# Kernel optimization log

Hardware: AMD Instinct MI355X
Metric: run time of the kernel (lower is better)

The kernel has to match this reference:

```python
import jax, jax.numpy as jnp
import numpy as np

N = 10000      # nodes
E = 80000      # directed edges (before self loops)
F_IN = 128     # input feature dim
OUT = 16       # out_channels (classes)


def setup_inputs() -> dict:
    key = jax.random.key(0)
    ks = jax.random.split(key, 20)
    p = lambda k, shape: (jax.random.normal(k, shape, jnp.float32) * 0.1)
    x = jax.random.normal(ks[0], (N, F_IN), jnp.float32)
    edge_index = jax.random.randint(ks[1], (2, E), 0, N, dtype=jnp.int64)
    return {
        "x": x, "edge_index": edge_index,
        # conv1: in=128 -> heads=10, ch=256
        "W1": p(ks[2], (F_IN, 10 * 256)), "as1": p(ks[3], (10, 256)), "ad1": p(ks[4], (10, 256)), "b1": jnp.zeros((10 * 256,), jnp.float32),
        # conv2: in=2560 -> heads=8, ch=56
        "W2": p(ks[5], (2560, 8 * 56)), "as2": p(ks[6], (8, 56)), "ad2": p(ks[7], (8, 56)), "b2": jnp.zeros((8 * 56,), jnp.float32),
        # conv3: in=448 -> heads=4, ch=32
        "W3": p(ks[8], (448, 4 * 32)), "as3": p(ks[9], (4, 32)), "ad3": p(ks[10], (4, 32)), "b3": jnp.zeros((4 * 32,), jnp.float32),
        # conv4: in=128 -> heads=1, ch=OUT, concat=False (mean over heads)
        "W4": p(ks[11], (128, 1 * OUT)), "as4": p(ks[12], (1, OUT)), "ad4": p(ks[13], (1, OUT)), "b4": jnp.zeros((OUT,), jnp.float32),
    }


def _gat_layer(x, src, dst, W, a_src, a_dst, b, heads, ch, concat, n):
    # linear projection -> [n, H, C]
    h = (x @ W).reshape(n, heads, ch)
    # per-node attention halves (PyG decomposition of a^T [h_i || h_j])
    e_src = jnp.einsum('nhc,hc->nh', h, a_src)
    e_dst = jnp.einsum('nhc,hc->nh', h, a_dst)
    # per-edge logits, LeakyReLU(0.2) as in PyG GATConv
    e = jax.nn.leaky_relu(e_src[src] + e_dst[dst], 0.2)  # [E', H]
    # segment softmax over edges grouped by destination node
    m = jax.ops.segment_max(e, dst, num_segments=n)
    m = jnp.where(jnp.isfinite(m), m, 0.0)
    ex = jnp.exp(e - m[dst])
    denom = jax.ops.segment_sum(ex, dst, num_segments=n)
    alpha = ex / (denom[dst] + 1e-16)  # [E', H]
    # weighted scatter-sum of source messages
    out = jax.ops.segment_sum(alpha[:, :, None] * h[src], dst, num_segments=n)  # [n, H, C]
    out = out.reshape(n, heads * ch) if concat else out.mean(axis=1)
    return out + b


def reference(x, edge_index, W1, as1, ad1, b1, W2, as2, ad2, b2,
              W3, as3, ad3, b3, W4, as4, ad4, b4):
    n = x.shape[0]
    loops = jnp.arange(n, dtype=edge_index.dtype)
    src = jnp.concatenate([edge_index[0], loops])  # add_self_loops=True
    dst = jnp.concatenate([edge_index[1], loops])
    lrelu = lambda t: jax.nn.leaky_relu(t, 0.1)  # outer activations in forward()
    h = lrelu(_gat_layer(x, src, dst, W1, as1, ad1, b1, 10, 256, True, n))
    h = lrelu(_gat_layer(h, src, dst, W2, as2, ad2, b2, 8, 56, True, n))
    h = lrelu(_gat_layer(h, src, dst, W3, as3, ad3, b3, 4, 32, True, n))
    h = lrelu(_gat_layer(h, src, dst, W4, as4, ad4, b4, 1, OUT, False, n))
    return jax.nn.softmax(h, axis=1)
```

## Files before the change

kernel.cpp:

```cpp
#include <hip/hip_runtime.h>
#include <math.h>

#define NNODES 10000
#define MPAD   10112
#define NEDGES 80000
#define ETOT   (NEDGES + NNODES)

typedef __attribute__((ext_vector_type(4))) float f32x4;
typedef __attribute__((ext_vector_type(8))) short bf16x8;
typedef __attribute__((ext_vector_type(4))) unsigned int u32x4;

__device__ inline unsigned short f2bf(float f) {
    unsigned int u = __float_as_uint(f);
    unsigned int r = (u + 0x7fffu + ((u >> 16) & 1u)) >> 16;
    return (unsigned short)r;
}
__device__ inline float bf2f(unsigned short h) {
    return __uint_as_float(((unsigned int)h) << 16);
}
__device__ inline float lrelu01(float v) { return (v > 0.f) ? v : 0.1f * v; }
__device__ inline float lrelu02(float v) { return (v > 0.f) ? v : 0.2f * v; }

__global__ void count_deg(const int* __restrict__ ei, int* __restrict__ indeg,
                          int E, int n) {
    int i = blockIdx.x * blockDim.x + threadIdx.x;
    if (i >= E + n) return;
    int dst = (i < E) ? ei[E + i] : (i - E);
    atomicAdd(&indeg[dst], 1);
}

__global__ void scan_rowptr(const int* __restrict__ indeg, int* __restrict__ row_ptr,
                            int* __restrict__ cursor, int n) {
    __shared__ int sums[1024];
    int tid = threadIdx.x;
    int per = (n + 1023) / 1024;
    int start = tid * per;
    int end = start + per; if (end > n) end = n;
    int s = 0;
    for (int i = start; i < end; ++i) s += indeg[i];
    sums[tid] = s;
    __syncthreads();
    for (int off = 1; off < 1024; off <<= 1) {
        int v = (tid >= off) ? sums[tid - off] : 0;
        __syncthreads();
        sums[tid] += v;
        __syncthreads();
    }
    int excl = (tid == 0) ? 0 : sums[tid - 1];
    for (int i = start; i < end; ++i) {
        row_ptr[i] = excl;
        cursor[i]  = excl;
        excl += indeg[i];
    }
    if (tid == 1023) row_ptr[n] = sums[1023];
}

__global__ void scatter_edges(const int* __restrict__ ei, int* __restrict__ cursor,
                              int* __restrict__ col, int E, int n) {
    int i = blockIdx.x * blockDim.x + threadIdx.x;
    if (i >= E + n) return;
    int src, dst;
    if (i < E) { src = ei[i]; dst = ei[E + i]; }
    else       { src = i - E; dst = i - E; }
    int pos = atomicAdd(&cursor[dst], 1);
    col[pos] = src;
}

__global__ void convert_bf16(const float* __restrict__ in, unsigned short* __restrict__ out,
                             int n) {
    int i = blockIdx.x * blockDim.x + threadIdx.x;
    if (i < n) out[i] = f2bf(in[i]);
}

__global__ void transpose_all(const float* __restrict__ W1, const float* __restrict__ W2,
                              const float* __restrict__ W3,
                              unsigned short* __restrict__ W1t,
                              unsigned short* __restrict__ W2t,
                              unsigned short* __restrict__ W3t) {
    __shared__ float t[32][33];
    int b = blockIdx.x;
    const float* W; unsigned short* Wt; int K, N, nb, kb;
    if (b < 320)       { W = W1; Wt = W1t; K = 128;  N = 2560; int i = b;        nb = i % 80; kb = i / 80; }
    else if (b < 1440) { W = W2; Wt = W2t; K = 2560; N = 448;  int i = b - 320;  nb = i % 14; kb = i / 14; }
    else               { W = W3; Wt = W3t; K = 448;  N = 128;  int i = b - 1440; nb = i % 4;  kb = i / 4;  }
    int kb32 = kb * 32, nb32 = nb * 32;
    int tx = threadIdx.x, ty = threadIdx.y;
    #pragma unroll
    for (int i = 0; i < 32; i += 8)
        t[ty + i][tx] = W[(size_t)(kb32 + ty + i) * N + nb32 + tx];
    __syncthreads();
    #pragma unroll
    for (int i = 0; i < 32; i += 8)
        Wt[(size_t)(nb32 + ty + i) * K + kb32 + tx] = f2bf(t[tx][ty + i]);
}

__global__ void make_wsd(const float* __restrict__ W1, const float* __restrict__ as1,
                         const float* __restrict__ ad1,
                         float* __restrict__ wsrc, float* __restrict__ wdst) {
    int idx = blockIdx.x * blockDim.x + threadIdx.x;
    if (idx >= 1280) return;
    int h = idx >> 7, k = idx & 127;
    const float* wrow = W1 + (size_t)k * 2560 + h * 256;
    const float* as = as1 + h * 256;
    const float* ad = ad1 + h * 256;
    float s = 0.f, d = 0.f;
    for (int c = 0; c < 256; c += 4) {
        f32x4 w = *(const f32x4*)&wrow[c];
        f32x4 a = *(const f32x4*)&as[c];
        f32x4 b = *(const f32x4*)&ad[c];
        #pragma unroll
        for (int j = 0; j < 4; ++j) { s += w[j] * a[j]; d += w[j] * b[j]; }
    }
    wsrc[h * 128 + k] = s;
    wdst[h * 128 + k] = d;
}

__global__ __launch_bounds__(256) void e1_dots(const unsigned short* __restrict__ xb,
                                               const float* __restrict__ wsrc,
                                               const float* __restrict__ wdst,
                                               float* __restrict__ e_src,
                                               float* __restrict__ e_dst, int M) {
    __shared__ float ws[1280], wd[1280];
    int tid = threadIdx.x;
    for (int i = tid; i < 1280; i += 256) { ws[i] = wsrc[i]; wd[i] = wdst[i]; }
    __syncthreads();
    int node = blockIdx.x * 4 + (tid >> 6);
    int lane = tid & 63;
    if (node >= M) return;
    unsigned int xv = ((const unsigned int*)xb)[node * 64 + lane];
    float v0 = bf2f((unsigned short)(xv & 0xffffu));
    float v1 = bf2f((unsigned short)(xv >> 16));
    #pragma unroll
    for (int h = 0; h < 10; ++h) {
        float ps = v0 * ws[h * 128 + 2 * lane] + v1 * ws[h * 128 + 2 * lane + 1];
        float pd = v0 * wd[h * 128 + 2 * lane] + v1 * wd[h * 128 + 2 * lane + 1];
        #pragma unroll
        for (int off = 32; off; off >>= 1) {
            ps += __shfl_down(ps, off);
            pd += __shfl_down(pd, off);
        }
        if (lane == 0) { e_src[node * 10 + h] = ps; e_dst[node * 10 + h] = pd; }
    }
}

__global__ __launch_bounds__(64) void agg_x(const unsigned short* __restrict__ xb,
                                            const float* __restrict__ e_src,
                                            const float* __restrict__ e_dst,
                                            const int* __restrict__ row_ptr,
                                            const int* __restrict__ col,
                                            unsigned short* __restrict__ xagg) {
    int node = blockIdx.x;
    int lane = threadIdx.x;
    int rs = row_ptr[node], re = row_ptr[node + 1];
    float edv = (lane < 10) ? e_dst[node * 10 + lane] : 0.f;

    float dn = 0.f;
    float a0[10], a1[10];
    #pragma unroll
    for (int h = 0; h < 10; ++h) { a0[h] = 0.f; a1[h] = 0.f; }
    for (int i = rs; i < re; ++i) {
        int s = col[i];
        float w = 0.f;
        if (lane < 10) w = __expf(lrelu02(e_src[s * 10 + lane] + edv));
        dn += w;
        unsigned int xv = ((const unsigned int*)xb)[s * 64 + lane];
        float v0 = bf2f((unsigned short)(xv & 0xffffu));
        float v1 = bf2f((unsigned short)(xv >> 16));
        #pragma unroll
        for (int h = 0; h < 10; ++h) {
            float wh = __shfl(w, h);
            a0[h] += wh * v0;
            a1[h] += wh * v1;
        }
    }
    #pragma unroll
    for (int h = 0; h < 10; ++h) {
        float rdn = 1.f / (__shfl(dn, h) + 1e-16f);
        unsigned int o = (unsigned int)f2bf(a0[h] * rdn) |
                         ((unsigned int)f2bf(a1[h] * rdn) << 16);
        ((unsigned int*)xagg)[((size_t)node * 10 + h) * 64 + lane] = o;
    }
}


#define GBM 128
#define GBK 32
__global__ __launch_bounds__(256) void gemm_l1(const unsigned short* __restrict__ A,
                                               const unsigned short* __restrict__ Bt,
                                               const float* __restrict__ bias,
                                               unsigned short* __restrict__ C) {
    constexpr int NT = 128, NI = 4, K = 128;
    __shared__ short As[GBM * GBK];
    __shared__ short Bs[NT * GBK];
    int h  = blockIdx.x >> 1;
    int nt = blockIdx.x & 1;
    int bn = h * 256 + nt * 128;
    int bm = blockIdx.y * GBM;
    int tid  = threadIdx.x;
    int wave = tid >> 6, lane = tid & 63;
    int wr = wave >> 1, wc = wave & 1;
    int lrow  = lane >> 2;
    int lk    = (((lane & 3) ^ ((lrow >> 1) & 3))) * 8;
    int row16 = lane & 15;
    int qs    = (((lane >> 4) ^ ((row16 >> 1) & 3))) * 8;

    f32x4 acc[4][NI];
    #pragma unroll
    for (int mi = 0; mi < 4; ++mi)
        #pragma unroll
        for (int ni = 0; ni < NI; ++ni) acc[mi][ni] = (f32x4){0.f, 0.f, 0.f, 0.f};

    for (int k0 = 0; k0 < K; k0 += GBK) {
        #pragma unroll
        for (int i = 0; i < 2; ++i) {
            int c = i * 4 + wave;
            int row = c * 16 + lrow;
            const unsigned short* gp = A + ((size_t)(bm + row) * 10 + h) * K + k0 + lk;
            __builtin_amdgcn_global_load_lds(
                (const __attribute__((address_space(1))) void*)gp,
                (__attribute__((address_space(3))) void*)&As[c * 512], 16, 0, 0);
        }
        #pragma unroll
        for (int i = 0; i < 2; ++i) {
            int c = i * 4 + wave;
            int row = c * 16 + lrow;
            const unsigned short* gp = Bt + (size_t)(bn + row) * K + k0 + lk;
            __builtin_amdgcn_global_load_lds(
                (const __attribute__((address_space(1))) void*)gp,
                (__attribute__((address_space(3))) void*)&Bs[c * 512], 16, 0, 0);
        }
        __syncthreads();
        bf16x8 af[4], bfr[NI];
        #pragma unroll
        for (int mi = 0; mi < 4; ++mi)
            af[mi] = *(const bf16x8*)&As[(wr * 64 + mi * 16 + row16) * GBK + qs];
        #pragma unroll
        for (int ni = 0; ni < NI; ++ni)
            bfr[ni] = *(const bf16x8*)&Bs[(wc * 64 + ni * 16 + row16) * GBK + qs];
        #pragma unroll
        for (int mi = 0; mi < 4; ++mi)
            #pragma unroll
            for (int ni = 0; ni < NI; ++ni)
                acc[mi][ni] = __builtin_amdgcn_mfma_f32_16x16x32_bf16(
                    af[mi], bfr[ni], acc[mi][ni], 0, 0, 0);
        __syncthreads();
    }

    int rbase = bm + wr * 64 + (lane >> 4) * 4;
    #pragma unroll
    for (int mi = 0; mi < 4; ++mi)
        #pragma unroll
        for (int ni = 0; ni < NI; ++ni) {
            int cc = bn + wc * 64 + ni * 16 + (lane & 15);
            float b = bias[cc];
            #pragma unroll
            for (int r = 0; r < 4; ++r) {
                float v = lrelu01(acc[mi][ni][r] + b);
                C[(size_t)(rbase + mi * 16 + r) * 2560 + cc] = f2bf(v);
            }
        }
}

template <int NT, bool SWIZ>
__global__ __launch_bounds__(256) void gemm_mfma(const unsigned short* __restrict__ A,
                                                 const unsigned short* __restrict__ Bt,
                                                 unsigned short* __restrict__ C,
                                                 int N, int nbn, int K, int klen) {
    constexpr int NI = NT / 32;
    __shared__ short As[GBM * GBK];
    __shared__ short Bs[NT * GBK];
    int bn, bm, kbeg, kend;
    size_t zoff = 0;
    if constexpr (SWIZ) {
        int b = blockIdx.x;
        int x = b & 7, t = b >> 3;
        int j = x + 8 * (t / nbn);
        if (j >= MPAD / GBM) return;
        bn = (t % nbn) * NT;
        bm = j * GBM;
        kbeg = blockIdx.y * klen;
        kend = kbeg + klen;
        zoff = (size_t)blockIdx.y * MPAD * N;
    } else {
        bn = blockIdx.x * NT;
        bm = blockIdx.y * GBM;
        kbeg = 0; kend = K;
    }
    int tid  = threadIdx.x;
    int wave = tid >> 6, lane = tid & 63;
    int wr = wave >> 1, wc = wave & 1;
    int lrow  = lane >> 2;
    int lk    = (((lane & 3) ^ ((lrow >> 1) & 3))) * 8;
    int row16 = lane & 15;
    int qs    = (((lane >> 4) ^ ((row16 >> 1) & 3))) * 8;

    f32x4 acc[4][NI];
    #pragma unroll
    for (int mi = 0; mi < 4; ++mi)
        #pragma unroll
        for (int ni = 0; ni < NI; ++ni) acc[mi][ni] = (f32x4){0.f, 0.f, 0.f, 0.f};

    for (int k0 = kbeg; k0 < kend; k0 += GBK) {
        #pragma unroll
        for (int i = 0; i < 2; ++i) {
            int c = i * 4 + wave;
            int row = c * 16 + lrow;
            const unsigned short* gp = A + (size_t)(bm + row) * K + k0 + lk;
            __builtin_amdgcn_global_load_lds(
                (const __attribute__((address_space(1))) void*)gp,
                (__attribute__((address_space(3))) void*)&As[c * 512], 16, 0, 0);
        }
        #pragma unroll
        for (int i = 0; i < NT / 64; ++i) {
            int c = i * 4 + wave;
            int row = c * 16 + lrow;
            const unsigned short* gp = Bt + (size_t)(bn + row) * K + k0 + lk;
            __builtin_amdgcn_global_load_lds(
                (const __attribute__((address_space(1))) void*)gp,
                (__attribute__((address_space(3))) void*)&Bs[c * 512], 16, 0, 0);
        }
        __syncthreads();
        bf16x8 af[4], bfr[NI];
        #pragma unroll
        for (int mi = 0; mi < 4; ++mi)
            af[mi] = *(const bf16x8*)&As[(wr * 64 + mi * 16 + row16) * GBK + qs];
        #pragma unroll
        for (int ni = 0; ni < NI; ++ni)
            bfr[ni] = *(const bf16x8*)&Bs[(wc * (NT / 2) + ni * 16 + row16) * GBK + qs];
        #pragma unroll
        for (int mi = 0; mi < 4; ++mi)
            #pragma unroll
            for (int ni = 0; ni < NI; ++ni)
                acc[mi][ni] = __builtin_amdgcn_mfma_f32_16x16x32_bf16(
                    af[mi], bfr[ni], acc[mi][ni], 0, 0, 0);
        __syncthreads();
    }

    int rbase = bm + wr * 64 + (lane >> 4) * 4;
    int cbase = bn + wc * (NT / 2) + (lane & 15);
    #pragma unroll
    for (int mi = 0; mi < 4; ++mi)
        #pragma unroll
        for (int ni = 0; ni < NI; ++ni)
            #pragma unroll
            for (int r = 0; r < 4; ++r)
                C[zoff + (size_t)(rbase + mi * 16 + r) * N + cbase + ni * 16] =
                    f2bf(acc[mi][ni][r]);
}

template <int S>
__global__ void reduce_k(const unsigned int* __restrict__ P, unsigned int* __restrict__ out,
                         size_t stride, int n2) {
    int i = blockIdx.x * blockDim.x + threadIdx.x;
    if (i >= n2) return;
    float lo = 0.f, hi = 0.f;
    #pragma unroll
    for (int s = 0; s < S; ++s) {
        unsigned int v = P[s * stride + i];
        lo += bf2f((unsigned short)(v & 0xffffu));
        hi += bf2f((unsigned short)(v >> 16));
    }
    out[i] = (unsigned int)f2bf(lo) | ((unsigned int)f2bf(hi) << 16);
}

__global__ __launch_bounds__(256) void gemm4_attn(const unsigned short* __restrict__ A,
                                                  const float* __restrict__ W,
                                                  const float* __restrict__ as4,
                                                  const float* __restrict__ ad4,
                                                  unsigned short* __restrict__ C,
                                                  float* __restrict__ e_src,
                                                  float* __restrict__ e_dst, int M) {
    __shared__ float Ws[128 * 16];
    int tid = threadIdx.x;
    for (int i = tid; i < 2048; i += 256) Ws[i] = W[i];
    __syncthreads();
    int node = blockIdx.x * 16 + (tid >> 4);
    int n = tid & 15;
    if (node >= M) return;
    const unsigned short* ap = A + (size_t)node * 128;
    float acc = 0.f;
    #pragma unroll 8
    for (int k = 0; k < 128; ++k)
        acc += bf2f(ap[k]) * Ws[k * 16 + n];
    C[(size_t)node * 16 + n] = f2bf(acc);
    float vs = acc * as4[n];
    float vd = acc * ad4[n];
    #pragma unroll
    for (int off = 1; off < 16; off <<= 1) {
        vs += __shfl_xor(vs, off);
        vd += __shfl_xor(vd, off);
    }
    if (n == 0) { e_src[node] = vs; e_dst[node] = vd; }
}

template <int H, int C>
__global__ __launch_bounds__(64) void attn_small(const unsigned short* __restrict__ h,
                                                 const float* __restrict__ a_src,
                                                 const float* __restrict__ a_dst,
                                                 float* __restrict__ e_src,
                                                 float* __restrict__ e_dst) {
    constexpr int LPH = 64 / H;
    constexpr int CPL = C / LPH;
    int node = blockIdx.x;
    int lane = threadIdx.x;
    int head = lane / LPH;
    int k = lane - head * LPH;
    const unsigned short* hp = h + (size_t)node * (H * C) + head * C + k * CPL;
    const float* as = a_src + head * C + k * CPL;
    const float* ad = a_dst + head * C + k * CPL;
    float s1 = 0.f, s2 = 0.f;
    #pragma unroll
    for (int c = 0; c < CPL; ++c) {
        float v = bf2f(hp[c]);
        s1 += v * as[c];
        s2 += v * ad[c];
    }
    #pragma unroll
    for (int off = LPH / 2; off; off >>= 1) {
        s1 += __shfl_down(s1, off);
        s2 += __shfl_down(s2, off);
    }
    if (k == 0) { e_src[node * H + head] = s1; e_dst[node * H + head] = s2; }
}

__global__ __launch_bounds__(64) void agg_l2(const unsigned short* __restrict__ h,
                                             const float* __restrict__ e_src,
                                             const float* __restrict__ e_dst,
                                             const int* __restrict__ row_ptr,
                                             const int* __restrict__ col,
                                             const float* __restrict__ bias,
                                             unsigned short* __restrict__ out) {
    const int H = 8;
    int node = blockIdx.x;
    int lane = threadIdx.x;
    bool act = lane < 56;
    int head = act ? (lane / 7) : 0;
    int cpos = act ? (lane - head * 7) : 0;
    int rs = row_ptr[node], re = row_ptr[node + 1];
    float edv = e_dst[node * H + head];

    float dn = 0.f;
    float acc0[8], acc1[8];
    #pragma unroll
    for (int k = 0; k < 8; ++k) { acc0[k] = 0.f; acc1[k] = 0.f; }
    int i = rs;
    for (; i + 1 < re; i += 2) {
        int s0 = col[i], s1 = col[i + 1];
        float es0 = e_src[s0 * H + head];
        float es1 = e_src[s1 * H + head];
        u32x4 hv0 = *(const u32x4*)(h + (size_t)s0 * 448 + head * 56 + cpos * 8);
        u32x4 hv1 = *(const u32x4*)(h + (size_t)s1 * 448 + head * 56 + cpos * 8);
        float w0 = __expf(lrelu02(es0 + edv));
        float w1 = __expf(lrelu02(es1 + edv));
        dn += w0 + w1;
        #pragma unroll
        for (int d = 0; d < 4; ++d) {
            acc0[2 * d]     += w0 * bf2f((unsigned short)(hv0[d] & 0xffffu));
            acc0[2 * d + 1] += w0 * bf2f((unsigned short)(hv0[d] >> 16));
            acc1[2 * d]     += w1 * bf2f((unsigned short)(hv1[d] & 0xffffu));
            acc1[2 * d + 1] += w1 * bf2f((unsigned short)(hv1[d] >> 16));
        }
    }
    if (i < re) {
        int s = col[i];
        float w = __expf(lrelu02(e_src[s * H + head] + edv));
        dn += w;
        u32x4 hv = *(const u32x4*)(h + (size_t)s * 448 + head * 56 + cpos * 8);
        #pragma unroll
        for (int d = 0; d < 4; ++d) {
            acc0[2 * d]     += w * bf2f((unsigned short)(hv[d] & 0xffffu));
            acc0[2 * d + 1] += w * bf2f((unsigned short)(hv[d] >> 16));
        }
    }
    float rdn = 1.f / (dn + 1e-16f);

    if (act) {
        const float* bp = bias + head * 56 + cpos * 8;
        u32x4 o;
        #pragma unroll
        for (int d = 0; d < 4; ++d) {
            float v0 = lrelu01((acc0[2 * d] + acc1[2 * d]) * rdn + bp[2 * d]);
            float v1 = lrelu01((acc0[2 * d + 1] + acc1[2 * d + 1]) * rdn + bp[2 * d + 1]);
            o[d] = (unsigned int)f2bf(v0) | ((unsigned int)f2bf(v1) << 16);
        }
        *(u32x4*)(out + (size_t)node * 448 + head * 56 + cpos * 8) = o;
    }
}

__global__ __launch_bounds__(64) void agg_l3(const unsigned short* __restrict__ h,
                                             const float* __restrict__ e_src,
                                             const float* __restrict__ e_dst,
                                             const int* __restrict__ row_ptr,
                                             const int* __restrict__ col,
                                             const float* __restrict__ bias,
                                             unsigned short* __restrict__ out) {
    const int H = 4;
    int node = blockIdx.x;
    int lane = threadIdx.x;
    bool act = lane < 16;
    int head = (lane >> 2) & 3;
    int cpos = lane & 3;
    int rs = row_ptr[node], re = row_ptr[node + 1];
    float edv = e_dst[node * H + head];

    float dn = 0.f;
    float acc0[8], acc1[8];
    #pragma unroll
    for (int k = 0; k < 8; ++k) { acc0[k] = 0.f; acc1[k] = 0.f; }
    int i = rs;
    for (; i + 1 < re; i += 2) {
        int s0 = col[i], s1 = col[i + 1];
        float es0 = e_src[s0 * H + head];
        float es1 = e_src[s1 * H + head];
        u32x4 hv0 = *(const u32x4*)(h + (size_t)s0 * 128 + head * 32 + cpos * 8);
        u32x4 hv1 = *(const u32x4*)(h + (size_t)s1 * 128 + head * 32 + cpos * 8);
        float w0 = __expf(lrelu02(es0 + edv));
        float w1 = __expf(lrelu02(es1 + edv));
        dn += w0 + w1;
        #pragma unroll
        for (int d = 0; d < 4; ++d) {
            acc0[2 * d]     += w0 * bf2f((unsigned short)(hv0[d] & 0xffffu));
            acc0[2 * d + 1] += w0 * bf2f((unsigned short)(hv0[d] >> 16));
            acc1[2 * d]     += w1 * bf2f((unsigned short)(hv1[d] & 0xffffu));
            acc1[2 * d + 1] += w1 * bf2f((unsigned short)(hv1[d] >> 16));
        }
    }
    if (i < re) {
        int s = col[i];
        float w = __expf(lrelu02(e_src[s * H + head] + edv));
        dn += w;
        u32x4 hv = *(const u32x4*)(h + (size_t)s * 128 + head * 32 + cpos * 8);
        #pragma unroll
        for (int d = 0; d < 4; ++d) {
            acc0[2 * d]     += w * bf2f((unsigned short)(hv[d] & 0xffffu));
            acc0[2 * d + 1] += w * bf2f((unsigned short)(hv[d] >> 16));
        }
    }
    float rdn = 1.f / (dn + 1e-16f);

    if (act) {
        const float* bp = bias + head * 32 + cpos * 8;
        u32x4 o;
        #pragma unroll
        for (int d = 0; d < 4; ++d) {
            float v0 = lrelu01((acc0[2 * d] + acc1[2 * d]) * rdn + bp[2 * d]);
            float v1 = lrelu01((acc0[2 * d + 1] + acc1[2 * d + 1]) * rdn + bp[2 * d + 1]);
            o[d] = (unsigned int)f2bf(v0) | ((unsigned int)f2bf(v1) << 16);
        }
        *(u32x4*)(out + (size_t)node * 128 + head * 32 + cpos * 8) = o;
    }
}

__global__ __launch_bounds__(64) void agg4_softmax(const unsigned int* __restrict__ h2,
                                                   const float* __restrict__ e_src,
                                                   const float* __restrict__ e_dst,
                                                   const int* __restrict__ row_ptr,
                                                   const int* __restrict__ col,
                                                   const float* __restrict__ bias,
                                                   float* __restrict__ out) {
    int node = blockIdx.x;
    int lane = threadIdx.x;
    int cpos = lane & 7;
    int rs = row_ptr[node], re = row_ptr[node + 1];
    float edv = e_dst[node];

    float dn = 0.f, a0 = 0.f, a1 = 0.f;
    for (int i = rs; i < re; ++i) {
        int s = col[i];
        float w = __expf(lrelu02(e_src[s] + edv));
        dn += w;
        unsigned int hv = h2[(size_t)s * 8 + cpos];
        a0 += w * bf2f((unsigned short)(hv & 0xffffu));
        a1 += w * bf2f((unsigned short)(hv >> 16));
    }
    float rdn = 1.f / (dn + 1e-16f);
    float v0 = lrelu01(a0 * rdn + bias[2 * cpos]);
    float v1 = lrelu01(a1 * rdn + bias[2 * cpos + 1]);

    float m = fmaxf(v0, v1);
    #pragma unroll
    for (int off = 4; off; off >>= 1) m = fmaxf(m, __shfl_xor(m, off));
    float e0 = __expf(v0 - m), e1 = __expf(v1 - m);
    float s = e0 + e1;
    #pragma unroll
    for (int off = 4; off; off >>= 1) s += __shfl_xor(s, off);
    float r = 1.f / s;
    if (lane < 8) {
        out[node * 16 + 2 * cpos]     = e0 * r;
        out[node * 16 + 2 * cpos + 1] = e1 * r;
    }
}

extern "C" void kernel_launch(void* const* d_in, const int* in_sizes, int n_in,
                              void* d_out, int out_size, void* d_ws, size_t ws_size,
                              hipStream_t stream) {
    const float* x   = (const float*)d_in[0];
    const int*   ei  = (const int*)d_in[1];
    const float* W1  = (const float*)d_in[2];
    const float* as1 = (const float*)d_in[3];
    const float* ad1 = (const float*)d_in[4];
    const float* b1  = (const float*)d_in[5];
    const float* W2  = (const float*)d_in[6];
    const float* as2 = (const float*)d_in[7];
    const float* ad2 = (const float*)d_in[8];
    const float* b2  = (const float*)d_in[9];
    const float* W3  = (const float*)d_in[10];
    const float* as3 = (const float*)d_in[11];
    const float* ad3 = (const float*)d_in[12];
    const float* b3  = (const float*)d_in[13];
    const float* W4  = (const float*)d_in[14];
    const float* as4 = (const float*)d_in[15];
    const float* ad4 = (const float*)d_in[16];
    const float* b4  = (const float*)d_in[17];

    char* ws = (char*)d_ws;
    size_t off = 0;
    auto alloc = [&](size_t bytes) -> void* {
        void* p = ws + off;
        off = (off + bytes + 255) & ~(size_t)255;
        return p;
    };
    unsigned short* hbuf = (unsigned short*)alloc((size_t)MPAD * 2560 * sizeof(short));
    unsigned short* abuf = (unsigned short*)alloc((size_t)MPAD * 2560 * sizeof(short));
    unsigned short* pbuf = (unsigned short*)alloc((size_t)4 * MPAD * 448 * sizeof(short));
    unsigned short* xagg = (unsigned short*)alloc((size_t)MPAD * 10 * 128 * sizeof(short));
    unsigned short* W1t  = (unsigned short*)alloc((size_t)2560 * 128 * sizeof(short));
    unsigned short* W2t  = (unsigned short*)alloc((size_t)448 * 2560 * sizeof(short));
    unsigned short* W3t  = (unsigned short*)alloc((size_t)128 * 448 * sizeof(short));
    float* wsrc   = (float*)alloc((size_t)10 * 128 * sizeof(float));
    float* wdst   = (float*)alloc((size_t)10 * 128 * sizeof(float));
    float* e_src  = (float*)alloc((size_t)NNODES * 10 * sizeof(float));
    float* e_dst  = (float*)alloc((size_t)NNODES * 10 * sizeof(float));
    int* indeg    = (int*)alloc(NNODES * sizeof(int));
    int* row_ptr  = (int*)alloc((NNODES + 1) * sizeof(int));
    int* cursor   = (int*)alloc(NNODES * sizeof(int));
    int* col      = (int*)alloc(ETOT * sizeof(int));
    (void)ws_size;

    hipMemsetAsync(indeg, 0, NNODES * sizeof(int), stream);
    int eb = (ETOT + 255) / 256;
    count_deg<<<eb, 256, 0, stream>>>(ei, indeg, NEDGES, NNODES);
    scan_rowptr<<<1, 1024, 0, stream>>>(indeg, row_ptr, cursor, NNODES);
    scatter_edges<<<eb, 256, 0, stream>>>(ei, cursor, col, NEDGES, NNODES);

    transpose_all<<<1496, dim3(32, 8), 0, stream>>>(W1, W2, W3, W1t, W2t, W3t);
    make_wsd<<<20, 64, 0, stream>>>(W1, as1, ad1, wsrc, wdst);
    convert_bf16<<<(NNODES * 128 + 255) / 256, 256, 0, stream>>>(x, abuf, NNODES * 128);

    const int Mb = MPAD / GBM;

    e1_dots<<<(NNODES + 3) / 4, 256, 0, stream>>>(abuf, wsrc, wdst, e_src, e_dst, NNODES);
    agg_x<<<NNODES, 64, 0, stream>>>(abuf, e_src, e_dst, row_ptr, col, xagg);
    gemm_l1<<<dim3(20, Mb), 256, 0, stream>>>(xagg, W1t, b1, abuf);

    gemm_mfma<64, true><<<dim3(8 * 7 * 10, 4), 256, 0, stream>>>(
        abuf, W2t, pbuf, 448, 7, 2560, 640);
    {
        int n2 = NNODES * 448 / 2;
        reduce_k<4><<<(n2 + 255) / 256, 256, 0, stream>>>(
            (const unsigned int*)pbuf, (unsigned int*)hbuf, (size_t)MPAD * 448 / 2, n2);
    }
    attn_small<8, 56><<<NNODES, 64, 0, stream>>>(hbuf, as2, ad2, e_src, e_dst);
    agg_l2<<<NNODES, 64, 0, stream>>>(hbuf, e_src, e_dst, row_ptr, col, b2, abuf);

    gemm_mfma<64, true><<<dim3(8 * 2 * 10, 2), 256, 0, stream>>>(
        abuf, W3t, pbuf, 128, 2, 448, 224);
    {
        int n2 = NNODES * 128 / 2;
        reduce_k<2><<<(n2 + 255) / 256, 256, 0, stream>>>(
            (const unsigned int*)pbuf, (unsigned int*)hbuf, (size_t)MPAD * 128 / 2, n2);
    }
    attn_small<4, 32><<<NNODES, 64, 0, stream>>>(hbuf, as3, ad3, e_src, e_dst);
    agg_l3<<<NNODES, 64, 0, stream>>>(hbuf, e_src, e_dst, row_ptr, col, b3, abuf);

    gemm4_attn<<<(NNODES + 15) / 16, 256, 0, stream>>>(
        abuf, W4, as4, ad4, hbuf, e_src, e_dst, NNODES);
    agg4_softmax<<<NNODES, 64, 0, stream>>>(
        (const unsigned int*)hbuf, e_src, e_dst, row_ptr, col, b4, (float*)d_out);
}
```

Baseline: 299.8 us.

## Merge prep kernels, widen GEMM K-tile to 64, fuse split-K reduce with attention

```diff
diff --git a/kernel.cpp b/kernel.cpp
--- a/kernel.cpp
+++ b/kernel.cpp
@@ -21,12 +21,71 @@
 __device__ inline float lrelu01(float v) { return (v > 0.f) ? v : 0.1f * v; }
 __device__ inline float lrelu02(float v) { return (v > 0.f) ? v : 0.2f * v; }
 
-__global__ void count_deg(const int* __restrict__ ei, int* __restrict__ indeg,
-                          int E, int n) {
-    int i = blockIdx.x * blockDim.x + threadIdx.x;
-    if (i >= E + n) return;
-    int dst = (i < E) ? ei[E + i] : (i - E);
-    atomicAdd(&indeg[dst], 1);
+__global__ __launch_bounds__(256) void prep_all(const int* __restrict__ ei,
+                                                int* __restrict__ indeg,
+                                                const float* __restrict__ x,
+                                                unsigned short* __restrict__ xb,
+                                                const float* __restrict__ W1,
+                                                const float* __restrict__ as1,
+                                                const float* __restrict__ ad1,
+                                                float* __restrict__ wsrc,
+                                                float* __restrict__ wdst,
+                                                const float* __restrict__ W2,
+                                                const float* __restrict__ W3,
+                                                unsigned short* __restrict__ W1t,
+                                                unsigned short* __restrict__ W2t,
+                                                unsigned short* __restrict__ W3t) {
+    __shared__ float t[32][33];
+    int b = blockIdx.x, tid = threadIdx.x;
+    if (b < 352) {
+        int i = b * 256 + tid;
+        if (i < ETOT) {
+            int dst = (i < NEDGES) ? ei[NEDGES + i] : (i - NEDGES);
+            atomicAdd(&indeg[dst], 1);
+        }
+        return;
+    }
+    b -= 352;
+    if (b < 5000) {
+        int i = b * 256 + tid;
+        if (i < NNODES * 128) xb[i] = f2bf(x[i]);
+        return;
+    }
+    b -= 5000;
+    if (b < 5) {
+        int idx = b * 256 + tid;
+        if (idx < 1280) {
+            int h = idx >> 7, k = idx & 127;
+            const float* wrow = W1 + (size_t)k * 2560 + h * 256;
+            const float* as = as1 + h * 256;
+            const float* ad = ad1 + h * 256;
+            float s = 0.f, d = 0.f;
+            for (int c = 0; c < 256; c += 4) {
+                f32x4 w = *(const f32x4*)&wrow[c];
+                f32x4 a = *(const f32x4*)&as[c];
+                f32x4 bb = *(const f32x4*)&ad[c];
+                #pragma unroll
+                for (int j = 0; j < 4; ++j) { s += w[j] * a[j]; d += w[j] * bb[j]; }
+            }
+            wsrc[h * 128 + k] = s;
+            wdst[h * 128 + k] = d;
+        }
+        return;
+    }
+    b -= 5;
+    const float* W; unsigned short* Wt; int K, N, nb, kb;
+    if (b < 320)       { W = W1; Wt = W1t; K = 128;  N = 2560; nb = b % 80; kb = b / 80; }
+    else if (b < 1440) { W = W2; Wt = W2t; K = 2560; N = 448;  int i = b - 320;  nb = i % 14; kb = i / 14; }
+    else               { W = W3; Wt = W3t; K = 448;  N = 128;  int i = b - 1440; nb = i % 4;  kb = i / 4;  }
+    int kb32 = kb * 32, nb32 = nb * 32;
+    int tx = tid & 31, ty = tid >> 5;
+    #pragma unroll
+    for (int i = 0; i < 32; i += 8)
+        t[ty + i][tx] = W[(size_t)(kb32 + ty + i) * N + nb32 + tx];
+    __syncthreads();
+    #pragma unroll
+    for (int i = 0; i < 32; i += 8)
+        Wt[(size_t)(nb32 + ty + i) * K + kb32 + tx] = f2bf(t[tx][ty + i]);
 }
 
 __global__ void scan_rowptr(const int* __restrict__ indeg, int* __restrict__ row_ptr,
@@ -55,78 +114,33 @@
     if (tid == 1023) row_ptr[n] = sums[1023];
 }
 
-__global__ void scatter_edges(const int* __restrict__ ei, int* __restrict__ cursor,
-                              int* __restrict__ col, int E, int n) {
-    int i = blockIdx.x * blockDim.x + threadIdx.x;
-    if (i >= E + n) return;
-    int src, dst;
-    if (i < E) { src = ei[i]; dst = ei[E + i]; }
-    else       { src = i - E; dst = i - E; }
-    int pos = atomicAdd(&cursor[dst], 1);
-    col[pos] = src;
-}
-
-__global__ void convert_bf16(const float* __restrict__ in, unsigned short* __restrict__ out,
-                             int n) {
-    int i = blockIdx.x * blockDim.x + threadIdx.x;
-    if (i < n) out[i] = f2bf(in[i]);
-}
-
-__global__ void transpose_all(const float* __restrict__ W1, const float* __restrict__ W2,
-                              const float* __restrict__ W3,
-                              unsigned short* __restrict__ W1t,
-                              unsigned short* __restrict__ W2t,
-                              unsigned short* __restrict__ W3t) {
-    __shared__ float t[32][33];
-    int b = blockIdx.x;
-    const float* W; unsigned short* Wt; int K, N, nb, kb;
-    if (b < 320)       { W = W1; Wt = W1t; K = 128;  N = 2560; int i = b;        nb = i % 80; kb = i / 80; }
-    else if (b < 1440) { W = W2; Wt = W2t; K = 2560; N = 448;  int i = b - 320;  nb = i % 14; kb = i / 14; }
-    else               { W = W3; Wt = W3t; K = 448;  N = 128;  int i = b - 1440; nb = i % 4;  kb = i / 4;  }
-    int kb32 = kb * 32, nb32 = nb * 32;
-    int tx = threadIdx.x, ty = threadIdx.y;
-    #pragma unroll
-    for (int i = 0; i < 32; i += 8)
-        t[ty + i][tx] = W[(size_t)(kb32 + ty + i) * N + nb32 + tx];
-    __syncthreads();
-    #pragma unroll
-    for (int i = 0; i < 32; i += 8)
-        Wt[(size_t)(nb32 + ty + i) * K + kb32 + tx] = f2bf(t[tx][ty + i]);
-}
-
-__global__ void make_wsd(const float* __restrict__ W1, const float* __restrict__ as1,
-                         const float* __restrict__ ad1,
-                         float* __restrict__ wsrc, float* __restrict__ wdst) {
-    int idx = blockIdx.x * blockDim.x + threadIdx.x;
-    if (idx >= 1280) return;
-    int h = idx >> 7, k = idx & 127;
-    const float* wrow = W1 + (size_t)k * 2560 + h * 256;
-    const float* as = as1 + h * 256;
-    const float* ad = ad1 + h * 256;
-    float s = 0.f, d = 0.f;
-    for (int c = 0; c < 256; c += 4) {
-        f32x4 w = *(const f32x4*)&wrow[c];
-        f32x4 a = *(const f32x4*)&as[c];
-        f32x4 b = *(const f32x4*)&ad[c];
-        #pragma unroll
-        for (int j = 0; j < 4; ++j) { s += w[j] * a[j]; d += w[j] * b[j]; }
-    }
-    wsrc[h * 128 + k] = s;
-    wdst[h * 128 + k] = d;
-}
-
-__global__ __launch_bounds__(256) void e1_dots(const unsigned short* __restrict__ xb,
-                                               const float* __restrict__ wsrc,
-                                               const float* __restrict__ wdst,
-                                               float* __restrict__ e_src,
-                                               float* __restrict__ e_dst, int M) {
+__global__ __launch_bounds__(256) void scatter_e1(const int* __restrict__ ei,
+                                                  int* __restrict__ cursor,
+                                                  int* __restrict__ col,
+                                                  const unsigned short* __restrict__ xb,
+                                                  const float* __restrict__ wsrc,
+                                                  const float* __restrict__ wdst,
+                                                  float* __restrict__ e_src,
+                                                  float* __restrict__ e_dst) {
     __shared__ float ws[1280], wd[1280];
-    int tid = threadIdx.x;
+    int b = blockIdx.x, tid = threadIdx.x;
+    if (b < 352) {
+        int i = b * 256 + tid;
+        if (i < ETOT) {
+            int src, dst;
+            if (i < NEDGES) { src = ei[i]; dst = ei[NEDGES + i]; }
+            else            { src = i - NEDGES; dst = i - NEDGES; }
+            int pos = atomicAdd(&cursor[dst], 1);
+            col[pos] = src;
+        }
+        return;
+    }
+    b -= 352;
     for (int i = tid; i < 1280; i += 256) { ws[i] = wsrc[i]; wd[i] = wdst[i]; }
     __syncthreads();
-    int node = blockIdx.x * 4 + (tid >> 6);
+    int node = b * 4 + (tid >> 6);
     int lane = tid & 63;
-    if (node >= M) return;
+    if (node >= NNODES) return;
     unsigned int xv = ((const unsigned int*)xb)[node * 64 + lane];
     float v0 = bf2f((unsigned short)(xv & 0xffffu));
     float v1 = bf2f((unsigned short)(xv >> 16));
@@ -184,14 +198,13 @@
 
 
 #define GBM 128
-#define GBK 32
 __global__ __launch_bounds__(256) void gemm_l1(const unsigned short* __restrict__ A,
                                                const unsigned short* __restrict__ Bt,
                                                const float* __restrict__ bias,
                                                unsigned short* __restrict__ C) {
     constexpr int NT = 128, NI = 4, K = 128;
-    __shared__ short As[GBM * GBK];
-    __shared__ short Bs[NT * GBK];
+    __shared__ short As[GBM * 64];
+    __shared__ short Bs[NT * 64];
     int h  = blockIdx.x >> 1;
     int nt = blockIdx.x & 1;
     int bn = h * 256 + nt * 128;
@@ -199,10 +212,10 @@
     int tid  = threadIdx.x;
     int wave = tid >> 6, lane = tid & 63;
     int wr = wave >> 1, wc = wave & 1;
-    int lrow  = lane >> 2;
-    int lk    = (((lane & 3) ^ ((lrow >> 1) & 3))) * 8;
-    int row16 = lane & 15;
-    int qs    = (((lane >> 4) ^ ((row16 >> 1) & 3))) * 8;
+    int lr8    = lane >> 3;
+    int gchunk = (lane & 7) ^ lr8;
+    int row16  = lane & 15;
+    int quad   = lane >> 4;
 
     f32x4 acc[4][NI];
     #pragma unroll
@@ -210,39 +223,44 @@
         #pragma unroll
         for (int ni = 0; ni < NI; ++ni) acc[mi][ni] = (f32x4){0.f, 0.f, 0.f, 0.f};
 
-    for (int k0 = 0; k0 < K; k0 += GBK) {
-        #pragma unroll
-        for (int i = 0; i < 2; ++i) {
-            int c = i * 4 + wave;
-            int row = c * 16 + lrow;
-            const unsigned short* gp = A + ((size_t)(bm + row) * 10 + h) * K + k0 + lk;
+    for (int k0 = 0; k0 < K; k0 += 64) {
+        #pragma unroll
+        for (int r = 0; r < 4; ++r) {
+            int cs = r * 4 + wave;
+            int row = cs * 8 + lr8;
+            const unsigned short* gp = A + ((size_t)(bm + row) * 10 + h) * K + k0 + gchunk * 8;
             __builtin_amdgcn_global_load_lds(
                 (const __attribute__((address_space(1))) void*)gp,
-                (__attribute__((address_space(3))) void*)&As[c * 512], 16, 0, 0);
-        }
-        #pragma unroll
-        for (int i = 0; i < 2; ++i) {
-            int c = i * 4 + wave;
-            int row = c * 16 + lrow;
-            const unsigned short* gp = Bt + (size_t)(bn + row) * K + k0 + lk;
+                (__attribute__((address_space(3))) void*)&As[cs * 512], 16, 0, 0);
+        }
+        #pragma unroll
+        for (int r = 0; r < 4; ++r) {
+            int cs = r * 4 + wave;
+            int row = cs * 8 + lr8;
+            const unsigned short* gp = Bt + (size_t)(bn + row) * K + k0 + gchunk * 8;
             __builtin_amdgcn_global_load_lds(
                 (const __attribute__((address_space(1))) void*)gp,
-                (__attribute__((address_space(3))) void*)&Bs[c * 512], 16, 0, 0);
+                (__attribute__((address_space(3))) void*)&Bs[cs * 512], 16, 0, 0);
         }
         __syncthreads();
-        bf16x8 af[4], bfr[NI];
-        #pragma unroll
-        for (int mi = 0; mi < 4; ++mi)
-            af[mi] = *(const bf16x8*)&As[(wr * 64 + mi * 16 + row16) * GBK + qs];
-        #pragma unroll
-        for (int ni = 0; ni < NI; ++ni)
-            bfr[ni] = *(const bf16x8*)&Bs[(wc * 64 + ni * 16 + row16) * GBK + qs];
-        #pragma unroll
-        for (int mi = 0; mi < 4; ++mi)
+        #pragma unroll
+        for (int kh = 0; kh < 2; ++kh) {
+            int q = kh * 4 + quad;
+            int pos = (q ^ (row16 & 7)) * 8;
+            bf16x8 af[4], bfr[NI];
+            #pragma unroll
+            for (int mi = 0; mi < 4; ++mi)
+                af[mi] = *(const bf16x8*)&As[(wr * 64 + mi * 16 + row16) * 64 + pos];
             #pragma unroll
             for (int ni = 0; ni < NI; ++ni)
-                acc[mi][ni] = __builtin_amdgcn_mfma_f32_16x16x32_bf16(
-                    af[mi], bfr[ni], acc[mi][ni], 0, 0, 0);
+                bfr[ni] = *(const bf16x8*)&Bs[(wc * 64 + ni * 16 + row16) * 64 + pos];
+            #pragma unroll
+            for (int mi = 0; mi < 4; ++mi)
+                #pragma unroll
+                for (int ni = 0; ni < NI; ++ni)
+                    acc[mi][ni] = __builtin_amdgcn_mfma_f32_16x16x32_bf16(
+                        af[mi], bfr[ni], acc[mi][ni], 0, 0, 0);
+        }
         __syncthreads();
     }
 
@@ -261,31 +279,108 @@
         }
 }
 
-template <int NT, bool SWIZ>
-__global__ __launch_bounds__(256) void gemm_mfma(const unsigned short* __restrict__ A,
-                                                 const unsigned short* __restrict__ Bt,
-                                                 unsigned short* __restrict__ C,
-                                                 int N, int nbn, int K, int klen) {
+template <int NT>
+__global__ __launch_bounds__(256) void gemm_k64(const unsigned short* __restrict__ A,
+                                                const unsigned short* __restrict__ Bt,
+                                                unsigned short* __restrict__ C,
+                                                int N, int nbn, int K, int klen) {
+    constexpr int NI = NT / 32;
+    __shared__ short As[GBM * 64];
+    __shared__ short Bs[NT * 64];
+    int b = blockIdx.x;
+    int x = b & 7, t = b >> 3;
+    int j = x + 8 * (t / nbn);
+    if (j >= MPAD / GBM) return;
+    int bn = (t % nbn) * NT;
+    int bm = j * GBM;
+    int kbeg = blockIdx.y * klen;
+    int kend = kbeg + klen;
+    size_t zoff = (size_t)blockIdx.y * MPAD * N;
+    int tid  = threadIdx.x;
+    int wave = tid >> 6, lane = tid & 63;
+    int wr = wave >> 1, wc = wave & 1;
+    int lr8    = lane >> 3;
+    int gchunk = (lane & 7) ^ lr8;
+    int row16  = lane & 15;
+    int quad   = lane >> 4;
+
+    f32x4 acc[4][NI];
+    #pragma unroll
+    for (int mi = 0; mi < 4; ++mi)
+        #pragma unroll
+        for (int ni = 0; ni < NI; ++ni) acc[mi][ni] = (f32x4){0.f, 0.f, 0.f, 0.f};
+
+    for (int k0 = kbeg; k0 < kend; k0 += 64) {
+        #pragma unroll
+        for (int r = 0; r < 4; ++r) {
+            int cs = r * 4 + wave;
+            int row = cs * 8 + lr8;
+            const unsigned short* gp = A + (size_t)(bm + row) * K + k0 + gchunk * 8;
+            __builtin_amdgcn_global_load_lds(
+                (const __attribute__((address_space(1))) void*)gp,
+                (__attribute__((address_space(3))) void*)&As[cs * 512], 16, 0, 0);
+        }
+        #pragma unroll
+        for (int r = 0; r < NT / 32; ++r) {
+            int cs = r * 4 + wave;
+            int row = cs * 8 + lr8;
+            const unsigned short* gp = Bt + (size_t)(bn + row) * K + k0 + gchunk * 8;
+            __builtin_amdgcn_global_load_lds(
+                (const __attribute__((address_space(1))) void*)gp,
+                (__attribute__((address_space(3))) void*)&Bs[cs * 512], 16, 0, 0);
+        }
+        __syncthreads();
+        #pragma unroll
+        for (int kh = 0; kh < 2; ++kh) {
+            int q = kh * 4 + quad;
+            int pos = (q ^ (row16 & 7)) * 8;
+            bf16x8 af[4], bfr[NI];
+            #pragma unroll
+            for (int mi = 0; mi < 4; ++mi)
+                af[mi] = *(const bf16x8*)&As[(wr * 64 + mi * 16 + row16) * 64 + pos];
+            #pragma unroll
+            for (int ni = 0; ni < NI; ++ni)
+                bfr[ni] = *(const bf16x8*)&Bs[(wc * (NT / 2) + ni * 16 + row16) * 64 + pos];
+            #pragma unroll
+            for (int mi = 0; mi < 4; ++mi)
+                #pragma unroll
+                for (int ni = 0; ni < NI; ++ni)
+                    acc[mi][ni] = __builtin_amdgcn_mfma_f32_16x16x32_bf16(
+                        af[mi], bfr[ni], acc[mi][ni], 0, 0, 0);
+        }
+        __syncthreads();
+    }
+
+    int rbase = bm + wr * 64 + (lane >> 4) * 4;
+    int cbase = bn + wc * (NT / 2) + (lane & 15);
+    #pragma unroll
+    for (int mi = 0; mi < 4; ++mi)
+        #pragma unroll
+        for (int ni = 0; ni < NI; ++ni)
+            #pragma unroll
+            for (int r = 0; r < 4; ++r)
+                C[zoff + (size_t)(rbase + mi * 16 + r) * N + cbase + ni * 16] =
+                    f2bf(acc[mi][ni][r]);
+}
+
+#define GBK 32
+template <int NT>
+__global__ __launch_bounds__(256) void gemm_k32(const unsigned short* __restrict__ A,
+                                                const unsigned short* __restrict__ Bt,
+                                                unsigned short* __restrict__ C,
+                                                int N, int nbn, int K, int klen) {
     constexpr int NI = NT / 32;
     __shared__ short As[GBM * GBK];
     __shared__ short Bs[NT * GBK];
-    int bn, bm, kbeg, kend;
-    size_t zoff = 0;
-    if constexpr (SWIZ) {
-        int b = blockIdx.x;
-        int x = b & 7, t = b >> 3;
-        int j = x + 8 * (t / nbn);
-        if (j >= MPAD / GBM) return;
-        bn = (t % nbn) * NT;
-        bm = j * GBM;
-        kbeg = blockIdx.y * klen;
-        kend = kbeg + klen;
-        zoff = (size_t)blockIdx.y * MPAD * N;
-    } else {
-        bn = blockIdx.x * NT;
-        bm = blockIdx.y * GBM;
-        kbeg = 0; kend = K;
-    }
+    int b = blockIdx.x;
+    int x = b & 7, t = b >> 3;
+    int j = x + 8 * (t / nbn);
+    if (j >= MPAD / GBM) return;
+    int bn = (t % nbn) * NT;
+    int bm = j * GBM;
+    int kbeg = blockIdx.y * klen;
+    int kend = kbeg + klen;
+    size_t zoff = (size_t)blockIdx.y * MPAD * N;
     int tid  = threadIdx.x;
     int wave = tid >> 6, lane = tid & 63;
     int wr = wave >> 1, wc = wave & 1;
@@ -348,19 +443,90 @@
                     f2bf(acc[mi][ni][r]);
 }
 
-template <int S>
-__global__ void reduce_k(const unsigned int* __restrict__ P, unsigned int* __restrict__ out,
-                         size_t stride, int n2) {
-    int i = blockIdx.x * blockDim.x + threadIdx.x;
-    if (i >= n2) return;
-    float lo = 0.f, hi = 0.f;
-    #pragma unroll
-    for (int s = 0; s < S; ++s) {
-        unsigned int v = P[s * stride + i];
-        lo += bf2f((unsigned short)(v & 0xffffu));
-        hi += bf2f((unsigned short)(v >> 16));
-    }
-    out[i] = (unsigned int)f2bf(lo) | ((unsigned int)f2bf(hi) << 16);
+__global__ __launch_bounds__(256) void reduce_attn_l2(const unsigned int* __restrict__ P,
+                                                      unsigned int* __restrict__ h2out,
+                                                      const float* __restrict__ as2,
+                                                      const float* __restrict__ ad2,
+                                                      float* __restrict__ e_src,
+                                                      float* __restrict__ e_dst, int M) {
+    const size_t stride = (size_t)MPAD * 224;
+    int wave = threadIdx.x >> 6, lane = threadIdx.x & 63;
+    int node = blockIdx.x * 4 + wave;
+    if (node >= M) return;
+    bool act = lane < 56;
+    int head = lane / 7;
+    int m = lane - head * 7;
+    size_t base = (size_t)node * 224 + lane * 4;
+    float lo[4], hi[4];
+    #pragma unroll
+    for (int d = 0; d < 4; ++d) {
+        float l = 0.f, hh = 0.f;
+        #pragma unroll
+        for (int s = 0; s < 4; ++s) {
+            unsigned int v = P[s * stride + base + d];
+            l  += bf2f((unsigned short)(v & 0xffffu));
+            hh += bf2f((unsigned short)(v >> 16));
+        }
+        lo[d] = l; hi[d] = hh;
+    }
+    if (act) {
+        #pragma unroll
+        for (int d = 0; d < 4; ++d)
+            h2out[base + d] = (unsigned int)f2bf(lo[d]) |
+                              ((unsigned int)f2bf(hi[d]) << 16);
+    }
+    float ps = 0.f, pd = 0.f;
+    if (act) {
+        const float* as = as2 + head * 56 + m * 8;
+        const float* ad = ad2 + head * 56 + m * 8;
+        #pragma unroll
+        for (int d = 0; d < 4; ++d) {
+            ps += lo[d] * as[2 * d] + hi[d] * as[2 * d + 1];
+            pd += lo[d] * ad[2 * d] + hi[d] * ad[2 * d + 1];
+        }
+    }
+    int lead = (lane / 7) * 7;
+    float ts = 0.f, td = 0.f;
+    #pragma unroll
+    for (int jj = 0; jj < 7; ++jj) {
+        int src = lead + jj; if (src > 63) src = 63;
+        ts += __shfl(ps, src);
+        td += __shfl(pd, src);
+    }
+    if (act && m == 0) {
+        e_src[node * 8 + head] = ts;
+        e_dst[node * 8 + head] = td;
+    }
+}
+
+__global__ __launch_bounds__(256) void reduce_attn_l3(const unsigned int* __restrict__ P,
+                                                      unsigned int* __restrict__ h2out,
+                                                      const float* __restrict__ as3,
+                                                      const float* __restrict__ ad3,
+                                                      float* __restrict__ e_src,
+                                                      float* __restrict__ e_dst, int M) {
+    const size_t stride = (size_t)MPAD * 64;
+    int wave = threadIdx.x >> 6, lane = threadIdx.x & 63;
+    int node = blockIdx.x * 4 + wave;
+    if (node >= M) return;
+    int head = lane >> 4;
+    int cl = (lane & 15) * 2;
+    size_t idx = (size_t)node * 64 + lane;
+    unsigned int v0 = P[idx], v1 = P[stride + idx];
+    float lo = bf2f((unsigned short)(v0 & 0xffffu)) + bf2f((unsigned short)(v1 & 0xffffu));
+    float hi = bf2f((unsigned short)(v0 >> 16)) + bf2f((unsigned short)(v1 >> 16));
+    h2out[idx] = (unsigned int)f2bf(lo) | ((unsigned int)f2bf(hi) << 16);
+    float ps = lo * as3[head * 32 + cl] + hi * as3[head * 32 + cl + 1];
+    float pd = lo * ad3[head * 32 + cl] + hi * ad3[head * 32 + cl + 1];
+    #pragma unroll
+    for (int off = 8; off; off >>= 1) {
+        ps += __shfl_xor(ps, off);
+        pd += __shfl_xor(pd, off);
+    }
+    if ((lane & 15) == 0) {
+        e_src[node * 4 + head] = ps;
+        e_dst[node * 4 + head] = pd;
+    }
 }
 
 __global__ __launch_bounds__(256) void gemm4_attn(const unsigned short* __restrict__ A,
@@ -391,36 +557,6 @@
         vd += __shfl_xor(vd, off);
     }
     if (n == 0) { e_src[node] = vs; e_dst[node] = vd; }
-}
-
-template <int H, int C>
-__global__ __launch_bounds__(64) void attn_small(const unsigned short* __restrict__ h,
-                                                 const float* __restrict__ a_src,
-                                                 const float* __restrict__ a_dst,
-                                                 float* __restrict__ e_src,
-                                                 float* __restrict__ e_dst) {
-    constexpr int LPH = 64 / H;
-    constexpr int CPL = C / LPH;
-    int node = blockIdx.x;
-    int lane = threadIdx.x;
-    int head = lane / LPH;
-    int k = lane - head * LPH;
-    const unsigned short* hp = h + (size_t)node * (H * C) + head * C + k * CPL;
-    const float* as = a_src + head * C + k * CPL;
-    const float* ad = a_dst + head * C + k * CPL;
-    float s1 = 0.f, s2 = 0.f;
-    #pragma unroll
-    for (int c = 0; c < CPL; ++c) {
-        float v = bf2f(hp[c]);
-        s1 += v * as[c];
-        s2 += v * ad[c];
-    }
-    #pragma unroll
-    for (int off = LPH / 2; off; off >>= 1) {
-        s1 += __shfl_down(s1, off);
-        s2 += __shfl_down(s2, off);
-    }
-    if (k == 0) { e_src[node * H + head] = s1; e_dst[node * H + head] = s2; }
 }
 
 __global__ __launch_bounds__(64) void agg_l2(const unsigned short* __restrict__ h,
@@ -638,39 +774,28 @@
     (void)ws_size;
 
     hipMemsetAsync(indeg, 0, NNODES * sizeof(int), stream);
-    int eb = (ETOT + 255) / 256;
-    count_deg<<<eb, 256, 0, stream>>>(ei, indeg, NEDGES, NNODES);
+
+    prep_all<<<352 + 5000 + 5 + 1496, 256, 0, stream>>>(
+        ei, indeg, x, abuf, W1, as1, ad1, wsrc, wdst, W2, W3, W1t, W2t, W3t);
     scan_rowptr<<<1, 1024, 0, stream>>>(indeg, row_ptr, cursor, NNODES);
-    scatter_edges<<<eb, 256, 0, stream>>>(ei, cursor, col, NEDGES, NNODES);
-
-    transpose_all<<<1496, dim3(32, 8), 0, stream>>>(W1, W2, W3, W1t, W2t, W3t);
-    make_wsd<<<20, 64, 0, stream>>>(W1, as1, ad1, wsrc, wdst);
-    convert_bf16<<<(NNODES * 128 + 255) / 256, 256, 0, stream>>>(x, abuf, NNODES * 128);
+    scatter_e1<<<352 + 2500, 256, 0, stream>>>(
+        ei, cursor, col, abuf, wsrc, wdst, e_src, e_dst);
 
     const int Mb = MPAD / GBM;
 
-    e1_dots<<<(NNODES + 3) / 4, 256, 0, stream>>>(abuf, wsrc, wdst, e_src, e_dst, NNODES);
     agg_x<<<NNODES, 64, 0, stream>>>(abuf, e_src, e_dst, row_ptr, col, xagg);
     gemm_l1<<<dim3(20, Mb), 256, 0, stream>>>(xagg, W1t, b1, abuf);
 
-    gemm_mfma<64, true><<<dim3(8 * 7 * 10, 4), 256, 0, stream>>>(
+    gemm_k64<64><<<dim3(8 * 7 * 10, 4), 256, 0, stream>>>(
         abuf, W2t, pbuf, 448, 7, 2560, 640);
-    {
-        int n2 = NNODES * 448 / 2;
-        reduce_k<4><<<(n2 + 255) / 256, 256, 0, stream>>>(
-            (const unsigned int*)pbuf, (unsigned int*)hbuf, (size_t)MPAD * 448 / 2, n2);
-    }
-    attn_small<8, 56><<<NNODES, 64, 0, stream>>>(hbuf, as2, ad2, e_src, e_dst);
+    reduce_attn_l2<<<2500, 256, 0, stream>>>(
+        (const unsigned int*)pbuf, (unsigned int*)hbuf, as2, ad2, e_src, e_dst, NNODES);
     agg_l2<<<NNODES, 64, 0, stream>>>(hbuf, e_src, e_dst, row_ptr, col, b2, abuf);
 
-    gemm_mfma<64, true><<<dim3(8 * 2 * 10, 2), 256, 0, stream>>>(
+    gemm_k32<64><<<dim3(8 * 2 * 10, 2), 256, 0, stream>>>(
         abuf, W3t, pbuf, 128, 2, 448, 224);
-    {
-        int n2 = NNODES * 128 / 2;
-        reduce_k<2><<<(n2 + 255) / 256, 256, 0, stream>>>(
-            (const unsigned int*)pbuf, (unsigned int*)hbuf, (size_t)MPAD * 128 / 2, n2);
-    }
-    attn_small<4, 32><<<NNODES, 64, 0, stream>>>(hbuf, as3, ad3, e_src, e_dst);
+    reduce_attn_l3<<<2500, 256, 0, stream>>>(
+        (const unsigned int*)pbuf, (unsigned int*)hbuf, as3, ad3, e_src, e_dst, NNODES);
     agg_l3<<<NNODES, 64, 0, stream>>>(hbuf, e_src, e_dst, row_ptr, col, b3, abuf);
 
     gemm4_attn<<<(NNODES + 15) / 16, 256, 0, stream>>>(
```

After: 281.5 us. 6.1% less time.
